# Kernel tuning notes

Hardware: AMD Instinct MI355X
Metric: run time of the kernel (lower is better)

Reference implementation:

```python
import jax, jax.numpy as jnp
import numpy as np
from jax import lax

EPS = 1e-4


def setup_inputs() -> dict:
    key = jax.random.key(0)
    k1, k2, k3 = jax.random.split(key, 3)
    B, L, M, D = 4, 4096, 1024, 2048
    chunked_states = jax.random.normal(k1, (B, M, D), dtype=jnp.float32)
    boundary_prob = jax.random.uniform(k2, (B, L, 2), dtype=jnp.float32)
    boundary_mask = jax.random.randint(k3, (B, L), 0, 2).astype(jnp.bool_)
    return {
        "chunked_states": chunked_states,
        "boundary_prob": boundary_prob,
        "boundary_mask": boundary_mask,
    }


def _ema_scan(x, p):
    """out[0]=x[0]; out[t]=p[t]*x[t]+(1-p[t])*out[t-1] via associative scan.
    x: (B,M,D), p: (B,M)."""
    a = (1.0 - p).at[:, 0].set(0.0)                 # (B, M)
    b = (p[..., None] * x).at[:, 0].set(x[:, 0])    # (B, M, D)

    def combine(c1, c2):
        a1, b1 = c1
        a2, b2 = c2
        return a1 * a2, a2[..., None] * b1 + b2

    _, out = lax.associative_scan(combine, (a, b), axis=1)
    return out


def reference(chunked_states, boundary_prob, boundary_mask):
    B, L = boundary_mask.shape
    M, D = chunked_states.shape[1], chunked_states.shape[2]

    p = jnp.clip(boundary_prob[..., -1].astype(jnp.float32), EPS, 1.0 - EPS)  # (B, L)

    # Stable-in-effect sort: boundary tokens keep index, non-boundary shifted by +L
    token_idx = jnp.arange(L, dtype=jnp.int32)[None, :] + (~boundary_mask).astype(jnp.int32) * L
    sorted_indices = jnp.argsort(token_idx, axis=1)[:, :M]                    # (B, M)
    p_chunked = jnp.take_along_axis(p, sorted_indices, axis=1)                # (B, M)

    expanded_chunked = _ema_scan(chunked_states, p_chunked)                   # (B, M, D)

    chunk_indices = jnp.clip(jnp.cumsum(boundary_mask.astype(jnp.int32), axis=1) - 1, 0, M - 1)  # (B, L)
    expanded_states = jnp.take_along_axis(expanded_chunked, chunk_indices[..., None], axis=1)    # (B, L, D)
    return expanded_states
```

## Files before the change

### kernel.cpp

```cpp
#include <hip/hip_runtime.h>

#define BB 4
#define LL 4096
#define MM 1024
#define DD 2048
#define SEG 128
#define SM 8
#define NSCAN (BB * SEG * 2)
#define BCAST 1024

typedef float f32x4 __attribute__((ext_vector_type(4)));

__global__ __launch_bounds__(1024) void prep_kernel(
    const float* __restrict__ bprob,
    const int*   __restrict__ bmask,
    float* __restrict__ p_chunked,
    int*   __restrict__ row_start,
    float* __restrict__ Ppref)
{
    const int b   = blockIdx.x;
    const int tid = threadIdx.x;
    const int lane = tid & 63;
    const int wid  = tid >> 6;

    __shared__ int wsum[16];
    __shared__ int s_total;
    __shared__ int rs_sh[MM + 1];

    rs_sh[tid] = LL;
    if (tid == 0) rs_sh[MM] = LL;

    int4 mv = reinterpret_cast<const int4*>(bmask + b * LL)[tid];
    int ms[4] = { mv.x, mv.y, mv.z, mv.w };
    int s = ms[0] + ms[1] + ms[2] + ms[3];

    int v = s;
    #pragma unroll
    for (int off = 1; off < 64; off <<= 1) {
        int u = __shfl_up(v, off, 64);
        if (lane >= off) v += u;
    }
    if (lane == 63) wsum[wid] = v;
    __syncthreads();
    if (tid == 0) {
        int acc = 0;
        #pragma unroll
        for (int w = 0; w < 16; ++w) { int t = wsum[w]; wsum[w] = acc; acc += t; }
        s_total = acc;
    }
    __syncthreads();

    const int NB = s_total;
    int e = (v - s) + wsum[wid];

    const int base_l = tid * 4;
    #pragma unroll
    for (int j = 0; j < 4; ++j) {
        int l = base_l + j;
        int m = ms[j];
        int incl = e + m;
        int ci = incl - 1;
        ci = ci < 0 ? 0 : (ci > MM - 1 ? MM - 1 : ci);
        int pci = e - 1;
        pci = pci < 0 ? 0 : (pci > MM - 1 ? MM - 1 : pci);
        if (l == 0 || ci != pci) rs_sh[ci] = l;
        int pos = m ? e : (NB + (l - e));
        if (pos < MM) {
            float2 pv = *reinterpret_cast<const float2*>(
                bprob + ((size_t)b * LL + l) * 2);
            float p = fminf(fmaxf(pv.y, 1e-4f), 1.0f - 1e-4f);
            p_chunked[b * MM + pos] = p;
        }
        e = incl;
    }
    __syncthreads();

    row_start[b * (MM + 1) + tid] = rs_sh[tid];
    if (tid == 0) row_start[b * (MM + 1) + MM] = rs_sh[MM];

    {
        int t = tid;
        float p = p_chunked[b * MM + t];
        float a = (t == 0) ? 0.0f : (1.0f - p);
        float pr = a;
        #pragma unroll
        for (int off = 1; off < SM; off <<= 1) {
            float u = __shfl_up(pr, off, SM);
            if ((t & (SM - 1)) >= off) pr *= u;
        }
        Ppref[b * MM + t] = pr;
    }
}

__global__ __launch_bounds__(256) void seglast_kernel(
    const float* __restrict__ x,
    const float* __restrict__ p_chunked,
    float* __restrict__ seglast)
{
    const int tid = threadIdx.x;
    const int d0  = blockIdx.x * 1024 + tid * 4;
    const int seg = blockIdx.y;
    const int b   = blockIdx.z;
    const int t0  = seg * SM;

    __shared__ float sp[SM];
    if (tid < SM) sp[tid] = p_chunked[b * MM + t0 + tid];
    __syncthreads();

    const size_t base = ((size_t)b * MM + t0) * DD + d0;

    f32x4 prev = {0.0f, 0.0f, 0.0f, 0.0f};
    #pragma unroll
    for (int i = 0; i < SM; ++i) {
        float p = sp[i];
        float ac, bc;
        if (i == 0) { ac = (seg == 0) ? 0.0f : (1.0f - p); bc = (seg == 0) ? 1.0f : p; }
        else        { ac = 1.0f - p; bc = p; }
        f32x4 xt = *reinterpret_cast<const f32x4*>(x + base + (size_t)i * DD);
        prev = ac * prev + bc * xt;
    }
    *reinterpret_cast<f32x4*>(seglast + ((size_t)b * SEG + seg) * DD + d0) = prev;
}

__global__ __launch_bounds__(256) void carry_kernel(
    float* __restrict__ buf,
    const float* __restrict__ Ppref,
    float* __restrict__ yM1)
{
    int idx = blockIdx.x * 256 + threadIdx.x;
    int b  = idx / (DD / 2);
    int d2 = (idx % (DD / 2)) * 2;

    float2 run = make_float2(0.0f, 0.0f);
    #pragma unroll 8
    for (int s = 0; s < SEG; ++s) {
        float* addr = buf + ((size_t)b * SEG + s) * DD + d2;
        float2 last = *reinterpret_cast<const float2*>(addr);
        *reinterpret_cast<float2*>(addr) = run;
        float Pf = Ppref[b * MM + s * SM + SM - 1];
        run.x = fmaf(Pf, run.x, last.x);
        run.y = fmaf(Pf, run.y, last.y);
    }
    *reinterpret_cast<float2*>(yM1 + (size_t)b * DD + d2) = run;
}

__global__ __launch_bounds__(256) void scatter_kernel(
    const float* __restrict__ x,
    const float* __restrict__ p_chunked,
    const int*   __restrict__ row_start,
    const float* __restrict__ carry,
    const float* __restrict__ yM1,
    float* __restrict__ out)
{
    const int id  = blockIdx.x;
    const int tid = threadIdx.x;

    if (id < NSCAN) {
        const int dsl = id & 1;
        const int seg = (id >> 1) & (SEG - 1);
        const int b   = id >> 8;
        const int d0  = dsl * 1024 + tid * 4;
        const int t0  = seg * SM;

        __shared__ float sp[SM];
        __shared__ int   rs[SM + 1];
        if (tid < SM) sp[tid] = p_chunked[b * MM + t0 + tid];
        if (tid < SM + 1) rs[tid] = row_start[b * (MM + 1) + t0 + tid];
        __syncthreads();

        f32x4 prev = *reinterpret_cast<const f32x4*>(
            carry + ((size_t)(b * SEG + seg)) * DD + d0);
        const size_t base = ((size_t)b * MM + t0) * DD + d0;

        #pragma unroll
        for (int i = 0; i < SM; ++i) {
            float p = sp[i];
            float ac, bc;
            if (i == 0) { ac = (seg == 0) ? 0.0f : (1.0f - p); bc = (seg == 0) ? 1.0f : p; }
            else        { ac = 1.0f - p; bc = p; }
            f32x4 xt = *reinterpret_cast<const f32x4*>(x + base + (size_t)i * DD);
            prev = ac * prev + bc * xt;

            int t = t0 + i;
            if (t == MM - 1) continue;
            int l0r = rs[i], l1r = rs[i + 1];
            for (int l = l0r; l < l1r; ++l)
                *reinterpret_cast<f32x4*>(out + ((size_t)b * LL + l) * DD + d0) = prev;
        }
    } else {
        const int j    = id - NSCAN;
        const int g    = j & 7;
        const int chnk = j >> 3;
        const int b    = g >> 1;
        const int dsl  = g & 1;
        const int d0   = dsl * 1024 + tid * 4;

        f32x4 v = *reinterpret_cast<const f32x4*>(yM1 + (size_t)b * DD + d0);
        const int l0 = row_start[b * (MM + 1) + (MM - 1)];
        for (int l = l0 + chnk; l < LL; l += 128)
            *reinterpret_cast<f32x4*>(out + ((size_t)b * LL + l) * DD + d0) = v;
    }
}

extern "C" void kernel_launch(void* const* d_in, const int* in_sizes, int n_in,
                              void* d_out, int out_size, void* d_ws, size_t ws_size,
                              hipStream_t stream) {
    const float* x     = (const float*)d_in[0];
    const float* bprob = (const float*)d_in[1];
    const int*   bmask = (const int*)d_in[2];

    float* out = (float*)d_out;

    float* buf       = (float*)d_ws;
    float* yM1       = buf + (size_t)BB * SEG * DD;
    float* p_chunked = yM1 + BB * DD;
    float* Ppref     = p_chunked + BB * MM;
    int*   row_start = (int*)(Ppref + BB * MM);

    prep_kernel<<<BB, 1024, 0, stream>>>(bprob, bmask, p_chunked, row_start, Ppref);
    seglast_kernel<<<dim3(DD / 1024, SEG, BB), 256, 0, stream>>>(x, p_chunked, buf);
    carry_kernel<<<(BB * DD / 2) / 256, 256, 0, stream>>>(buf, Ppref, yM1);
    scatter_kernel<<<NSCAN + BCAST, 256, 0, stream>>>(
        x, p_chunked, row_start, buf, yM1, out);
}
```

Before: 52.79 us.

## Replace sequential carry kernel with per-block decoupled lookback over segment tails

Removes the serial carry-propagation kernel and instead has each scatter block compute its incoming carry by walking backward over earlier segment end-states, weighting each by the running product of segment decay factors. The walk stops once that product falls below a small epsilon. This removes one launch and its long serial dependency chain, but every block now does redundant reads of earlier segment tails. The early exit relies on decay products shrinking and truncates contributions below the epsilon, which is an approximation.

```diff
diff --git a/kernel.cpp b/kernel.cpp
--- a/kernel.cpp
+++ b/kernel.cpp
@@ -8,6 +8,7 @@
 #define SM 8
 #define NSCAN (BB * SEG * 2)
 #define BCAST 1024
+#define EXIT_EPS 1e-7f
 
 typedef float f32x4 __attribute__((ext_vector_type(4)));
 
@@ -98,7 +99,8 @@
     float* __restrict__ seglast)
 {
     const int tid = threadIdx.x;
-    const int d0  = blockIdx.x * 1024 + tid * 4;
+    const int dsl = blockIdx.x;
+    const int d0  = dsl * 1024 + tid * 4;
     const int seg = blockIdx.y;
     const int b   = blockIdx.z;
     const int t0  = seg * SM;
@@ -119,41 +121,38 @@
         f32x4 xt = *reinterpret_cast<const f32x4*>(x + base + (size_t)i * DD);
         prev = ac * prev + bc * xt;
     }
-    *reinterpret_cast<f32x4*>(seglast + ((size_t)b * SEG + seg) * DD + d0) = prev;
-}
-
-__global__ __launch_bounds__(256) void carry_kernel(
-    float* __restrict__ buf,
-    const float* __restrict__ Ppref,
-    float* __restrict__ yM1)
-{
-    int idx = blockIdx.x * 256 + threadIdx.x;
-    int b  = idx / (DD / 2);
-    int d2 = (idx % (DD / 2)) * 2;
-
-    float2 run = make_float2(0.0f, 0.0f);
-    #pragma unroll 8
-    for (int s = 0; s < SEG; ++s) {
-        float* addr = buf + ((size_t)b * SEG + s) * DD + d2;
-        float2 last = *reinterpret_cast<const float2*>(addr);
-        *reinterpret_cast<float2*>(addr) = run;
-        float Pf = Ppref[b * MM + s * SM + SM - 1];
-        run.x = fmaf(Pf, run.x, last.x);
-        run.y = fmaf(Pf, run.y, last.y);
-    }
-    *reinterpret_cast<float2*>(yM1 + (size_t)b * DD + d2) = run;
+    *reinterpret_cast<f32x4*>(
+        seglast + (((size_t)(b * 2 + dsl) * SEG + seg)) * 1024 + tid * 4) = prev;
+}
+
+static __device__ __forceinline__ f32x4 lookback(
+    const float* __restrict__ seglast, const float* __restrict__ sPf,
+    int bd, int seg, int tid)
+{
+    f32x4 c = {0.0f, 0.0f, 0.0f, 0.0f};
+    float mult = 1.0f;
+    const float* base = seglast + (size_t)bd * SEG * 1024 + tid * 4;
+    for (int j = seg - 1; j >= 0; --j) {
+        f32x4 sl = *reinterpret_cast<const f32x4*>(base + (size_t)j * 1024);
+        c += mult * sl;
+        mult *= sPf[j];
+        if (mult < EXIT_EPS) break;
+    }
+    return c;
 }
 
 __global__ __launch_bounds__(256) void scatter_kernel(
     const float* __restrict__ x,
     const float* __restrict__ p_chunked,
+    const float* __restrict__ Ppref,
     const int*   __restrict__ row_start,
-    const float* __restrict__ carry,
-    const float* __restrict__ yM1,
+    const float* __restrict__ seglast,
     float* __restrict__ out)
 {
     const int id  = blockIdx.x;
     const int tid = threadIdx.x;
+
+    __shared__ float sPf[SEG];
 
     if (id < NSCAN) {
         const int dsl = id & 1;
@@ -161,17 +160,18 @@
         const int b   = id >> 8;
         const int d0  = dsl * 1024 + tid * 4;
         const int t0  = seg * SM;
+        const int bd  = b * 2 + dsl;
 
         __shared__ float sp[SM];
         __shared__ int   rs[SM + 1];
         if (tid < SM) sp[tid] = p_chunked[b * MM + t0 + tid];
         if (tid < SM + 1) rs[tid] = row_start[b * (MM + 1) + t0 + tid];
+        if (tid < SEG) sPf[tid] = Ppref[b * MM + tid * SM + SM - 1];
         __syncthreads();
 
-        f32x4 prev = *reinterpret_cast<const f32x4*>(
-            carry + ((size_t)(b * SEG + seg)) * DD + d0);
+        f32x4 prev = lookback(seglast, sPf, bd, seg, tid);
+
         const size_t base = ((size_t)b * MM + t0) * DD + d0;
-
         #pragma unroll
         for (int i = 0; i < SM; ++i) {
             float p = sp[i];
@@ -194,8 +194,13 @@
         const int b    = g >> 1;
         const int dsl  = g & 1;
         const int d0   = dsl * 1024 + tid * 4;
-
-        f32x4 v = *reinterpret_cast<const f32x4*>(yM1 + (size_t)b * DD + d0);
+        const int bd   = b * 2 + dsl;
+
+        if (tid < SEG) sPf[tid] = Ppref[b * MM + tid * SM + SM - 1];
+        __syncthreads();
+
+        f32x4 v = lookback(seglast, sPf, bd, SEG, tid);
+
         const int l0 = row_start[b * (MM + 1) + (MM - 1)];
         for (int l = l0 + chnk; l < LL; l += 128)
             *reinterpret_cast<f32x4*>(out + ((size_t)b * LL + l) * DD + d0) = v;
@@ -211,15 +216,13 @@
 
     float* out = (float*)d_out;
 
-    float* buf       = (float*)d_ws;
-    float* yM1       = buf + (size_t)BB * SEG * DD;
-    float* p_chunked = yM1 + BB * DD;
+    float* seglast   = (float*)d_ws;
+    float* p_chunked = seglast + (size_t)BB * 2 * SEG * 1024;
     float* Ppref     = p_chunked + BB * MM;
     int*   row_start = (int*)(Ppref + BB * MM);
 
     prep_kernel<<<BB, 1024, 0, stream>>>(bprob, bmask, p_chunked, row_start, Ppref);
-    seglast_kernel<<<dim3(DD / 1024, SEG, BB), 256, 0, stream>>>(x, p_chunked, buf);
-    carry_kernel<<<(BB * DD / 2) / 256, 256, 0, stream>>>(buf, Ppref, yM1);
+    seglast_kernel<<<dim3(2, SEG, BB), 256, 0, stream>>>(x, p_chunked, seglast);
     scatter_kernel<<<NSCAN + BCAST, 256, 0, stream>>>(
-        x, p_chunked, row_start, buf, yM1, out);
-}
+        x, p_chunked, Ppref, row_start, seglast, out);
+}
```

Result: faster. 44.21 us (-16.3%).
